# Optimization experiments

Measured on AMD Instinct MI355X. Metric: run time of the kernel, lower is better.

The kernel has to match this reference:

```python
import jax, jax.numpy as jnp
import numpy as np
import math

B, S_TGT, S_SRC, D, H, FF = 4, 2048, 2048, 512, 8, 2048
DK = D // H
EPS = 1e-6


def layernorm(x, gamma, mu):
    # torch: gamma*(x-mean)/(std+eps)+mu with unbiased std (ddof=1), eps OUTSIDE sqrt
    mean = jnp.mean(x, axis=-1, keepdims=True)
    std = jnp.std(x, axis=-1, keepdims=True, ddof=1)
    return gamma * (x - mean) / (std + EPS) + mu


def mha(q, k, v, wq, wk, wv, wo, bo, mask):
    # q:[B,Sq,D] k,v:[B,Sk,D]; weights [D,D] (applied as x@W)
    Bq, Sq, _ = q.shape
    Sk = k.shape[1]
    Q = (q @ wq).reshape(Bq, Sq, H, DK).transpose(0, 2, 1, 3)  # [B,H,Sq,dk]
    K = (k @ wk).reshape(Bq, Sk, H, DK).transpose(0, 2, 1, 3)
    V = (v @ wv).reshape(Bq, Sk, H, DK).transpose(0, 2, 1, 3)
    scores = jnp.einsum('bhqd,bhkd->bhqk', Q, K) / math.sqrt(DK)
    scores = jnp.where(mask == 0, -1e9, scores)
    attn = jax.nn.softmax(scores, axis=-1)
    out = jnp.einsum('bhqk,bhkd->bhqd', attn, V)  # [B,H,Sq,dk]
    out = out.transpose(0, 2, 1, 3).reshape(Bq, Sq, D)
    return out @ wo + bo


def setup_inputs() -> dict:
    key = jax.random.key(0)
    ks = jax.random.split(key, 20)
    sc = 0.02
    inp = {
        'x': jax.random.normal(ks[0], (B, S_TGT, D), jnp.float32),
        'encoder_output': jax.random.normal(ks[1], (B, S_SRC, D), jnp.float32),
        'src_mask': jnp.ones((1, 1, 1, S_SRC), jnp.int32),
        'tgt_mask': jnp.tril(jnp.ones((S_TGT, S_TGT), jnp.int32))[None, None],
        # self-attention params
        'sa_wq': jax.random.normal(ks[2], (D, D)) * sc,
        'sa_wk': jax.random.normal(ks[3], (D, D)) * sc,
        'sa_wv': jax.random.normal(ks[4], (D, D)) * sc,
        'sa_wo': jax.random.normal(ks[5], (D, D)) * sc,
        'sa_bo': jnp.zeros((D,), jnp.float32),
        # cross-attention params
        'ca_wq': jax.random.normal(ks[6], (D, D)) * sc,
        'ca_wk': jax.random.normal(ks[7], (D, D)) * sc,
        'ca_wv': jax.random.normal(ks[8], (D, D)) * sc,
        'ca_wo': jax.random.normal(ks[9], (D, D)) * sc,
        'ca_bo': jnp.zeros((D,), jnp.float32),
        # feed-forward params
        'ff_w1': jax.random.normal(ks[10], (D, FF)) * sc,
        'ff_b1': jnp.zeros((FF,), jnp.float32),
        'ff_w2': jax.random.normal(ks[11], (FF, D)) * sc,
        'ff_b2': jnp.zeros((D,), jnp.float32),
        # layernorm params (3 residual connections)
        'ln0_g': jnp.ones((D,), jnp.float32), 'ln0_b': jnp.zeros((D,), jnp.float32),
        'ln1_g': jnp.ones((D,), jnp.float32), 'ln1_b': jnp.zeros((D,), jnp.float32),
        'ln2_g': jnp.ones((D,), jnp.float32), 'ln2_b': jnp.zeros((D,), jnp.float32),
    }
    return inp


def reference(x, encoder_output, src_mask, tgt_mask,
              sa_wq, sa_wk, sa_wv, sa_wo, sa_bo,
              ca_wq, ca_wk, ca_wv, ca_wo, ca_bo,
              ff_w1, ff_b1, ff_w2, ff_b2,
              ln0_g, ln0_b, ln1_g, ln1_b, ln2_g, ln2_b):
    # pre-LN residual blocks; dropout in eval mode (identity)
    h = layernorm(x, ln0_g, ln0_b)
    x = x + mha(h, h, h, sa_wq, sa_wk, sa_wv, sa_wo, sa_bo, tgt_mask)
    h = layernorm(x, ln1_g, ln1_b)
    x = x + mha(h, encoder_output, encoder_output, ca_wq, ca_wk, ca_wv, ca_wo, ca_bo, src_mask)
    h = layernorm(x, ln2_g, ln2_b)
    ff = jax.nn.relu(h @ ff_w1 + ff_b1) @ ff_w2 + ff_b2
    return x + ff
```

## Files before the change

### kernel.cpp

```cpp
#include <hip/hip_runtime.h>
#include <cstdint>

typedef short s8v __attribute__((ext_vector_type(8)));
typedef short s4v __attribute__((ext_vector_type(4)));
typedef float f4v __attribute__((ext_vector_type(4)));
typedef unsigned int u32;

#define DEV static __device__ __forceinline__

DEV unsigned short f2bf(float f) {
  u32 u = __builtin_bit_cast(u32, f);
  u += 0x7FFF + ((u >> 16) & 1);
  return (unsigned short)(u >> 16);
}

DEV void gload16(const void* g, void* l) {
  __builtin_amdgcn_global_load_lds(
      (const __attribute__((address_space(1))) u32*)g,
      (__attribute__((address_space(3))) u32*)l, 16, 0, 0);
}

struct TransArgs {
  const float* in[10];
  unsigned short* out[10];
};

__global__ __launch_bounds__(256) void trans_all_kernel(TransArgs ta) {
  int id = blockIdx.x;
  int wi, t, K, N, tx, ty;
  if (id < 2048) {
    wi = id >> 8; t = id & 255; K = 512; N = 512; tx = t & 15; ty = t >> 4;
  } else if (id < 3072) {
    wi = 8; t = id - 2048; K = 512; N = 2048; tx = t & 63; ty = t >> 6;
  } else {
    wi = 9; t = id - 3072; K = 2048; N = 512; tx = t & 15; ty = t >> 4;
  }
  const float* in = ta.in[wi];
  unsigned short* out = ta.out[wi];
  __shared__ float tile[32][33];
  int lx = threadIdx.x & 31, ly = threadIdx.x >> 5;
  int bn = tx * 32, bk = ty * 32;
#pragma unroll
  for (int i = 0; i < 32; i += 8)
    tile[ly + i][lx] = in[(size_t)(bk + ly + i) * N + bn + lx];
  __syncthreads();
#pragma unroll
  for (int i = 0; i < 32; i += 8)
    out[(size_t)(bn + ly + i) * K + bk + lx] = f2bf(tile[lx][ly + i]);
}

__global__ __launch_bounds__(256) void cast_kernel(
    const float* __restrict__ in, unsigned short* __restrict__ out, int n8) {
  int i = blockIdx.x * 256 + threadIdx.x;
  if (i >= n8) return;
  const float4* p = (const float4*)(in + (size_t)i * 8);
  float4 a = p[0], b = p[1];
  float va[8] = {a.x, a.y, a.z, a.w, b.x, b.y, b.z, b.w};
  s8v o;
#pragma unroll
  for (int j = 0; j < 8; j++) o[j] = (short)f2bf(va[j]);
  *(s8v*)(out + (size_t)i * 8) = o;
}

__global__ __launch_bounds__(256) void ln_kernel(
    const float* __restrict__ x, const float* __restrict__ g,
    const float* __restrict__ bt, unsigned short* __restrict__ out) {
  int row = blockIdx.x * 4 + (threadIdx.x >> 6);
  int lane = threadIdx.x & 63;
  const float* xr = x + (size_t)row * 512 + lane * 8;
  float4 v0 = *(const float4*)xr;
  float4 v1 = *(const float4*)(xr + 4);
  float va[8] = {v0.x, v0.y, v0.z, v0.w, v1.x, v1.y, v1.z, v1.w};
  float s = 0.f, s2 = 0.f;
#pragma unroll
  for (int j = 0; j < 8; j++) { s += va[j]; s2 += va[j] * va[j]; }
#pragma unroll
  for (int off = 1; off < 64; off <<= 1) {
    s += __shfl_xor(s, off);
    s2 += __shfl_xor(s2, off);
  }
  float mean = s * (1.f / 512.f);
  float var = (s2 - 512.f * mean * mean) * (1.f / 511.f);
  var = fmaxf(var, 0.f);
  float inv = 1.f / (sqrtf(var) + 1e-6f);
  const float* gp = g + lane * 8;
  const float* bp = bt + lane * 8;
  float4 g0 = *(const float4*)gp, g1 = *(const float4*)(gp + 4);
  float4 b0 = *(const float4*)bp, b1 = *(const float4*)(bp + 4);
  float ga[8] = {g0.x, g0.y, g0.z, g0.w, g1.x, g1.y, g1.z, g1.w};
  float ba[8] = {b0.x, b0.y, b0.z, b0.w, b1.x, b1.y, b1.z, b1.w};
  s8v o;
#pragma unroll
  for (int j = 0; j < 8; j++)
    o[j] = (short)f2bf(ga[j] * (va[j] - mean) * inv + ba[j]);
  *(s8v*)(out + (size_t)row * 512 + lane * 8) = o;
}

#define EPI_QKV3 0
#define EPI_Q 1
#define EPI_KV2 2
#define EPI_BIAS_RES 3
#define EPI_RELU 4

template <int EPI, int BN>
__global__ __launch_bounds__(256, 3) void gemm_kernel(
    const unsigned short* __restrict__ A, const unsigned short* __restrict__ Bt,
    const float* __restrict__ bias, const float* __restrict__ res,
    void* __restrict__ out0, void* __restrict__ out1, void* __restrict__ out2,
    int M, int N, int K) {
  __shared__ alignas(16) unsigned short sA[2][128 * 32];
  __shared__ alignas(16) unsigned short sB[2][BN * 32];
  constexpr int NC = BN / 32;
  int tid = threadIdx.x;
  int w = tid >> 6, lane = tid & 63;
  int wm = w >> 1, wn = w & 1;
  int quad = lane >> 4, l15 = lane & 15;
  int bm = blockIdx.y * 128, bn = blockIdx.x * BN;

  int r0 = lane >> 2, c0 = (lane & 3) * 8;
  const unsigned short* gA0 = A + (size_t)(bm + w * 16 + r0) * K + c0;
  const unsigned short* gA1 = gA0 + (size_t)64 * K;
  const unsigned short* gB0 = Bt + (size_t)(bn + w * 16 + r0) * K + c0;
  const unsigned short* gB1 = gB0 + (size_t)64 * K;

  auto prefetch = [&](int k0, int buf) {
    gload16(gA0 + k0, &sA[buf][w * 512]);
    gload16(gA1 + k0, &sA[buf][(w + 4) * 512]);
    gload16(gB0 + k0, &sB[buf][w * 512]);
    if (BN == 128) gload16(gB1 + k0, &sB[buf][(w + 4) * 512]);
  };

  f4v acc[4][NC];
#pragma unroll
  for (int r = 0; r < 4; r++)
#pragma unroll
    for (int c = 0; c < NC; c++) acc[r][c] = {0.f, 0.f, 0.f, 0.f};

  prefetch(0, 0);
  int nk = K >> 5;
  for (int it = 0; it < nk; it++) {
    int buf = it & 1;
    __syncthreads();
    if (it + 1 < nk) prefetch((it + 1) << 5, buf ^ 1);
    s8v af[4], bf[NC];
#pragma unroll
    for (int r = 0; r < 4; r++)
      af[r] = *(const s8v*)&sA[buf][(wm * 64 + r * 16 + l15) * 32 + quad * 8];
#pragma unroll
    for (int c = 0; c < NC; c++)
      bf[c] = *(const s8v*)&sB[buf][(wn * (BN / 2) + c * 16 + l15) * 32 + quad * 8];
#pragma unroll
    for (int r = 0; r < 4; r++)
#pragma unroll
      for (int c = 0; c < NC; c++)
        acc[r][c] = __builtin_amdgcn_mfma_f32_16x16x32_bf16(af[r], bf[c], acc[r][c], 0, 0, 0);
  }

  constexpr int BP = 512 / BN;
  int route = 0;
  if (EPI == EPI_QKV3) route = blockIdx.x / BP;
  if (EPI == EPI_KV2) route = 1 + blockIdx.x / BP;
#pragma unroll
  for (int r = 0; r < 4; r++) {
#pragma unroll
    for (int c = 0; c < NC; c++) {
#pragma unroll
      for (int i = 0; i < 4; i++) {
        int row = bm + wm * 64 + r * 16 + quad * 4 + i;
        int col = bn + wn * (BN / 2) + c * 16 + l15;
        float v = acc[r][c][i];
        if (EPI == EPI_BIAS_RES) {
          float* o = (float*)out0;
          o[(size_t)row * N + col] = v + bias[col] + res[(size_t)row * N + col];
        } else if (EPI == EPI_RELU) {
          unsigned short* o = (unsigned short*)out0;
          o[(size_t)row * N + col] = f2bf(fmaxf(v + bias[col], 0.f));
        } else {
          int colq = col & 511;
          int b = row >> 11, s = row & 2047, h = colq >> 6, dk = colq & 63;
          if (route == 0) {
            unsigned short* o = (unsigned short*)out0;
            o[(((size_t)(b * 8 + h) * 2048) + s) * 64 + dk] = f2bf(v * 0.125f);
          } else if (route == 1) {
            unsigned short* o = (unsigned short*)out1;
            o[(((size_t)(b * 8 + h) * 2048) + s) * 64 + dk] = f2bf(v);
          } else {
            unsigned short* o = (unsigned short*)out2;
            o[(((size_t)(b * 8 + h) * 64) + dk) * 2048 + s] = f2bf(v);
          }
        }
      }
    }
  }
}

template <int CAUSAL>
__global__ __launch_bounds__(256, 2) void attn_kernel(
    const unsigned short* __restrict__ Q, const unsigned short* __restrict__ Kk,
    const unsigned short* __restrict__ Vt,
    unsigned short* __restrict__ out) {
  const int S = 2048;
  __shared__ alignas(16) unsigned short sK[2][64 * 64];
  __shared__ alignas(16) unsigned short sV[2][64 * 64];
  __shared__ alignas(16) unsigned short sO[128 * 68];
  int bh = blockIdx.x;
  int qt = CAUSAL ? ((int)gridDim.y - 1 - blockIdx.y) : blockIdx.y;
  int b = bh >> 3, h = bh & 7;
  int tid = threadIdx.x;
  int w = tid >> 6, lane = tid & 63;
  int quad = lane >> 4, l15 = lane & 15;

  const unsigned short* Qp = Q + (size_t)bh * S * 64;
  const unsigned short* Kp = Kk + (size_t)bh * S * 64;
  const unsigned short* Vp = Vt + (size_t)bh * 64 * S;

  s8v bq[2][2];
#pragma unroll
  for (int qb = 0; qb < 2; qb++) {
    const unsigned short* qr =
        Qp + (size_t)(qt * 128 + w * 32 + qb * 16 + l15) * 64 + quad * 8;
    bq[qb][0] = *(const s8v*)qr;
    bq[qb][1] = *(const s8v*)(qr + 32);
  }

  int rowA = ((l15 >> 2) * 8) + (l15 & 3);
  int koff[2][2][2];
#pragma unroll
  for (int win = 0; win < 2; win++)
#pragma unroll
    for (int half = 0; half < 2; half++) {
      int row = win * 32 + half * 4 + rowA;
      int h7 = (row & 7) ^ (((row >> 3) & 1) << 2);
      koff[win][half][0] = row * 64 + ((quad ^ h7) << 3);
      koff[win][half][1] = row * 64 + (((4 + quad) ^ h7) << 3);
    }
  int voff[4][2];
#pragma unroll
  for (int c2 = 0; c2 < 4; c2++) {
    int row = c2 * 16 + l15;
    int h7 = (row & 7) ^ (((row >> 3) & 1) << 2);
#pragma unroll
    for (int win = 0; win < 2; win++)
      voff[c2][win] = row * 64 + ((((win * 4) + quad) ^ h7) << 3);
  }
  int st_row[2], st_lds[2], st_cc[2];
#pragma unroll
  for (int c = 0; c < 2; c++) {
    int row = c * 32 + (tid >> 3), cc = tid & 7;
    int slot = cc ^ (row & 7) ^ (((row >> 3) & 1) << 2);
    st_row[c] = row;
    st_cc[c] = cc;
    st_lds[c] = row * 64 + slot * 8;
  }

  float l_lane[2] = {0.f, 0.f};
  f4v oacc[2][4];
#pragma unroll
  for (int qb = 0; qb < 2; qb++)
#pragma unroll
    for (int c2 = 0; c2 < 4; c2++) oacc[qb][c2] = {0.f, 0.f, 0.f, 0.f};

  int ntiles = CAUSAL ? (2 * qt + 2) : (S / 64);

  s8v kreg[2], vreg[2];
  auto load_t = [&](int t) {
    int kb = t * 64;
#pragma unroll
    for (int c = 0; c < 2; c++) {
      kreg[c] = *(const s8v*)(Kp + (size_t)(kb + st_row[c]) * 64 + st_cc[c] * 8);
      vreg[c] = *(const s8v*)(Vp + (size_t)st_row[c] * S + kb + st_cc[c] * 8);
    }
  };
  auto write_t = [&](int buf) {
#pragma unroll
    for (int c = 0; c < 2; c++) {
      *(s8v*)&sK[buf][st_lds[c]] = kreg[c];
      *(s8v*)&sV[buf][st_lds[c]] = vreg[c];
    }
  };

  load_t(0);
  write_t(0);

  for (int t = 0; t < ntiles; t++) {
    int buf = t & 1;
    __syncthreads();
    if (t + 1 < ntiles) load_t(t + 1);

    f4v sacc[2][2][2];
#pragma unroll
    for (int qb = 0; qb < 2; qb++)
#pragma unroll
      for (int win = 0; win < 2; win++)
#pragma unroll
        for (int half = 0; half < 2; half++) sacc[qb][win][half] = {0.f, 0.f, 0.f, 0.f};
#pragma unroll
    for (int win = 0; win < 2; win++)
#pragma unroll
      for (int half = 0; half < 2; half++) {
        s8v a0 = *(const s8v*)&sK[buf][koff[win][half][0]];
        s8v a1 = *(const s8v*)&sK[buf][koff[win][half][1]];
#pragma unroll
        for (int qb = 0; qb < 2; qb++) {
          sacc[qb][win][half] =
              __builtin_amdgcn_mfma_f32_16x16x32_bf16(a0, bq[qb][0], sacc[qb][win][half], 0, 0, 0);
          sacc[qb][win][half] =
              __builtin_amdgcn_mfma_f32_16x16x32_bf16(a1, bq[qb][1], sacc[qb][win][half], 0, 0, 0);
        }
      }

    if (CAUSAL && t >= 2 * qt) {
      int toff = (t - 2 * qt) * 64;
#pragma unroll
      for (int qb = 0; qb < 2; qb++) {
        int qloc = w * 32 + qb * 16 + l15;
#pragma unroll
        for (int win = 0; win < 2; win++)
#pragma unroll
          for (int half = 0; half < 2; half++)
#pragma unroll
            for (int i = 0; i < 4; i++)
              if (toff + win * 32 + quad * 8 + half * 4 + i > qloc)
                sacc[qb][win][half][i] = -1e9f;
      }
    }

    s8v bp[2][2];
#pragma unroll
    for (int qb = 0; qb < 2; qb++)
#pragma unroll
      for (int win = 0; win < 2; win++) {
        float p[8];
#pragma unroll
        for (int half = 0; half < 2; half++)
#pragma unroll
          for (int i = 0; i < 4; i++) {
            float e = __expf(sacc[qb][win][half][i]);
            p[half * 4 + i] = e;
            l_lane[qb] += e;
          }
        int4 pk;
#pragma unroll
        for (int j = 0; j < 4; j++)
          pk[j] = (int)__builtin_amdgcn_perm(
              __builtin_bit_cast(u32, p[2 * j + 1]),
              __builtin_bit_cast(u32, p[2 * j]), 0x07060302u);
        bp[qb][win] = __builtin_bit_cast(s8v, pk);
      }

#pragma unroll
    for (int c2 = 0; c2 < 4; c2++)
#pragma unroll
      for (int win = 0; win < 2; win++) {
        s8v av = *(const s8v*)&sV[buf][voff[c2][win]];
#pragma unroll
        for (int qb = 0; qb < 2; qb++)
          oacc[qb][c2] =
              __builtin_amdgcn_mfma_f32_16x16x32_bf16(av, bp[qb][win], oacc[qb][c2], 0, 0, 0);
      }

    if (t + 1 < ntiles) write_t(buf ^ 1);
  }

#pragma unroll
  for (int qb = 0; qb < 2; qb++) {
    float l = l_lane[qb];
    l += __shfl_xor(l, 16);
    l += __shfl_xor(l, 32);
    float inv = 1.f / l;
#pragma unroll
    for (int c2 = 0; c2 < 4; c2++) {
      s4v o;
#pragma unroll
      for (int i = 0; i < 4; i++) o[i] = (short)f2bf(oacc[qb][c2][i] * inv);
      *(s4v*)&sO[(w * 32 + qb * 16 + l15) * 68 + c2 * 16 + quad * 4] = o;
    }
  }
  __syncthreads();
#pragma unroll
  for (int c = 0; c < 4; c++) {
    int idx = c * 256 + tid;
    int r = idx >> 3, ch = idx & 7;
    s8v v = *(const s8v*)&sO[r * 68 + ch * 8];
    *(s8v*)(out + ((size_t)(b * S + qt * 128 + r) * 512) + h * 64 + ch * 8) = v;
  }
}

extern "C" void kernel_launch(void* const* d_in, const int* in_sizes, int n_in,
                              void* d_out, int out_size, void* d_ws, size_t ws_size,
                              hipStream_t stream) {
  const float* x = (const float*)d_in[0];
  const float* enc = (const float*)d_in[1];
  const float* sa_wq = (const float*)d_in[4];
  const float* sa_wk = (const float*)d_in[5];
  const float* sa_wv = (const float*)d_in[6];
  const float* sa_wo = (const float*)d_in[7];
  const float* sa_bo = (const float*)d_in[8];
  const float* ca_wq = (const float*)d_in[9];
  const float* ca_wk = (const float*)d_in[10];
  const float* ca_wv = (const float*)d_in[11];
  const float* ca_wo = (const float*)d_in[12];
  const float* ca_bo = (const float*)d_in[13];
  const float* ff_w1 = (const float*)d_in[14];
  const float* ff_b1 = (const float*)d_in[15];
  const float* ff_w2 = (const float*)d_in[16];
  const float* ff_b2 = (const float*)d_in[17];
  const float* ln0_g = (const float*)d_in[18];
  const float* ln0_b = (const float*)d_in[19];
  const float* ln1_g = (const float*)d_in[20];
  const float* ln1_b = (const float*)d_in[21];
  const float* ln2_g = (const float*)d_in[22];
  const float* ln2_b = (const float*)d_in[23];
  float* out = (float*)d_out;

  const int M = 8192;

  size_t off = 0;
  auto carve = [&](size_t bytes) -> void* {
    void* r = (char*)d_ws + off;
    off += (bytes + 255) & ~(size_t)255;
    return r;
  };
  unsigned short* swqT = (unsigned short*)carve(512 * 512 * 2);
  unsigned short* swkT = (unsigned short*)carve(512 * 512 * 2);
  unsigned short* swvT = (unsigned short*)carve(512 * 512 * 2);
  unsigned short* swoT = (unsigned short*)carve(512 * 512 * 2);
  unsigned short* cwqT = (unsigned short*)carve(512 * 512 * 2);
  unsigned short* cwkT = (unsigned short*)carve(512 * 512 * 2);
  unsigned short* cwvT = (unsigned short*)carve(512 * 512 * 2);
  unsigned short* cwoT = (unsigned short*)carve(512 * 512 * 2);
  unsigned short* w1T = (unsigned short*)carve((size_t)2048 * 512 * 2);
  unsigned short* w2T = (unsigned short*)carve((size_t)512 * 2048 * 2);
  unsigned short* enc_bf = (unsigned short*)carve((size_t)M * 512 * 2);
  unsigned short* h_bf = (unsigned short*)carve((size_t)M * 512 * 2);
  unsigned short* Qb = (unsigned short*)carve((size_t)M * 512 * 2);
  unsigned short* Kb = (unsigned short*)carve((size_t)M * 512 * 2);
  unsigned short* Vtb = (unsigned short*)carve((size_t)M * 512 * 2);
  unsigned short* attn_bf = (unsigned short*)carve((size_t)M * 512 * 2);
  float* x1 = (float*)carve((size_t)M * 512 * 4);
  unsigned short* f1 = (unsigned short*)carve((size_t)M * 2048 * 2);

  dim3 blk(256);

  TransArgs ta;
  ta.in[0] = sa_wq; ta.out[0] = swqT;
  ta.in[1] = sa_wk; ta.out[1] = swkT;
  ta.in[2] = sa_wv; ta.out[2] = swvT;
  ta.in[3] = sa_wo; ta.out[3] = swoT;
  ta.in[4] = ca_wq; ta.out[4] = cwqT;
  ta.in[5] = ca_wk; ta.out[5] = cwkT;
  ta.in[6] = ca_wv; ta.out[6] = cwvT;
  ta.in[7] = ca_wo; ta.out[7] = cwoT;
  ta.in[8] = ff_w1; ta.out[8] = w1T;
  ta.in[9] = ff_w2; ta.out[9] = w2T;
  trans_all_kernel<<<dim3(4096), blk, 0, stream>>>(ta);
  cast_kernel<<<dim3(M * 512 / 8 / 256), blk, 0, stream>>>(enc, enc_bf, M * 512 / 8);

  dim3 gProj(8, 64);
  dim3 gQKV(12, 64);
  dim3 gKV(16, 64);
  dim3 gFF1(16, 64);
  dim3 gAttn(32, 16);
  dim3 gLN(M / 4);

  ln_kernel<<<gLN, blk, 0, stream>>>(x, ln0_g, ln0_b, h_bf);
  gemm_kernel<EPI_QKV3, 128><<<gQKV, blk, 0, stream>>>(h_bf, swqT, nullptr, nullptr, Qb, Kb, Vtb, M, 1536, 512);
  attn_kernel<1><<<gAttn, blk, 0, stream>>>(Qb, Kb, Vtb, attn_bf);
  gemm_kernel<EPI_BIAS_RES, 64><<<gProj, blk, 0, stream>>>(attn_bf, swoT, sa_bo, x, x1, nullptr, nullptr, M, 512, 512);

  ln_kernel<<<gLN, blk, 0, stream>>>(x1, ln1_g, ln1_b, h_bf);
  gemm_kernel<EPI_Q, 64><<<gProj, blk, 0, stream>>>(h_bf, cwqT, nullptr, nullptr, Qb, nullptr, nullptr, M, 512, 512);
  gemm_kernel<EPI_KV2, 64><<<gKV, blk, 0, stream>>>(enc_bf, cwkT, nullptr, nullptr, nullptr, Kb, Vtb, M, 1024, 512);
  attn_kernel<0><<<gAttn, blk, 0, stream>>>(Qb, Kb, Vtb, attn_bf);
  gemm_kernel<EPI_BIAS_RES, 64><<<gProj, blk, 0, stream>>>(attn_bf, cwoT, ca_bo, x1, x1, nullptr, nullptr, M, 512, 512);

  ln_kernel<<<gLN, blk, 0, stream>>>(x1, ln2_g, ln2_b, h_bf);
  gemm_kernel<EPI_RELU, 128><<<gFF1, blk, 0, stream>>>(h_bf, w1T, ff_b1, nullptr, f1, nullptr, nullptr, M, 2048, 512);
  gemm_kernel<EPI_BIAS_RES, 64><<<gProj, blk, 0, stream>>>(f1, w2T, ff_b2, x1, out, nullptr, nullptr, M, 512, 2048);
}
```

Measured before the change: 415.6 us.

## Deepen attention K/V register prefetch, use exp2 softmax, swizzle GEMM blocks per XCD

The attention loop now keeps two register sets of K/V tiles and is unrolled by two, so global loads are issued two tiles ahead and more memory latency is hidden. The Q scale folds in log2(e), which lets softmax use exp2 in place of expf. The GEMM block index is remapped so consecutive row tiles are grouped per XCD, aiming for better L2 reuse of the A rows. The cost is higher register pressure in the attention kernel. The two-tile loop also assumes ntiles is even, which holds for the causal and full cases here.

```diff
diff --git a/kernel.cpp b/kernel.cpp
--- a/kernel.cpp
+++ b/kernel.cpp
@@ -101,6 +101,8 @@
 #define EPI_KV2 2
 #define EPI_BIAS_RES 3
 #define EPI_RELU 4
+
+#define QSCALE 0.18033688f
 
 template <int EPI, int BN>
 __global__ __launch_bounds__(256, 3) void gemm_kernel(
@@ -115,7 +117,12 @@
   int w = tid >> 6, lane = tid & 63;
   int wm = w >> 1, wn = w & 1;
   int quad = lane >> 4, l15 = lane & 15;
-  int bm = blockIdx.y * 128, bn = blockIdx.x * BN;
+
+  int lin = blockIdx.x + gridDim.x * blockIdx.y;
+  int xcd = lin & 7, j = lin >> 3;
+  int bmi = xcd * 8 + (j & 7);
+  int bni = j >> 3;
+  int bm = bmi * 128, bn = bni * BN;
 
   int r0 = lane >> 2, c0 = (lane & 3) * 8;
   const unsigned short* gA0 = A + (size_t)(bm + w * 16 + r0) * K + c0;
@@ -158,8 +165,8 @@
 
   constexpr int BP = 512 / BN;
   int route = 0;
-  if (EPI == EPI_QKV3) route = blockIdx.x / BP;
-  if (EPI == EPI_KV2) route = 1 + blockIdx.x / BP;
+  if (EPI == EPI_QKV3) route = bni / BP;
+  if (EPI == EPI_KV2) route = 1 + bni / BP;
 #pragma unroll
   for (int r = 0; r < 4; r++) {
 #pragma unroll
@@ -180,7 +187,7 @@
           int b = row >> 11, s = row & 2047, h = colq >> 6, dk = colq & 63;
           if (route == 0) {
             unsigned short* o = (unsigned short*)out0;
-            o[(((size_t)(b * 8 + h) * 2048) + s) * 64 + dk] = f2bf(v * 0.125f);
+            o[(((size_t)(b * 8 + h) * 2048) + s) * 64 + dk] = f2bf(v * QSCALE);
           } else if (route == 1) {
             unsigned short* o = (unsigned short*)out1;
             o[(((size_t)(b * 8 + h) * 2048) + s) * 64 + dk] = f2bf(v);
@@ -262,31 +269,24 @@
 
   int ntiles = CAUSAL ? (2 * qt + 2) : (S / 64);
 
-  s8v kreg[2], vreg[2];
-  auto load_t = [&](int t) {
+  s8v rk[2][2], rv[2][2];
+  auto load_set = [&](int t, int set) {
     int kb = t * 64;
 #pragma unroll
     for (int c = 0; c < 2; c++) {
-      kreg[c] = *(const s8v*)(Kp + (size_t)(kb + st_row[c]) * 64 + st_cc[c] * 8);
-      vreg[c] = *(const s8v*)(Vp + (size_t)st_row[c] * S + kb + st_cc[c] * 8);
+      rk[set][c] = *(const s8v*)(Kp + (size_t)(kb + st_row[c]) * 64 + st_cc[c] * 8);
+      rv[set][c] = *(const s8v*)(Vp + (size_t)st_row[c] * S + kb + st_cc[c] * 8);
     }
   };
-  auto write_t = [&](int buf) {
+  auto write_set = [&](int buf, int set) {
 #pragma unroll
     for (int c = 0; c < 2; c++) {
-      *(s8v*)&sK[buf][st_lds[c]] = kreg[c];
-      *(s8v*)&sV[buf][st_lds[c]] = vreg[c];
+      *(s8v*)&sK[buf][st_lds[c]] = rk[set][c];
+      *(s8v*)&sV[buf][st_lds[c]] = rv[set][c];
     }
   };
 
-  load_t(0);
-  write_t(0);
-
-  for (int t = 0; t < ntiles; t++) {
-    int buf = t & 1;
-    __syncthreads();
-    if (t + 1 < ntiles) load_t(t + 1);
-
+  auto compute = [&](int buf, int t) {
     f4v sacc[2][2][2];
 #pragma unroll
     for (int qb = 0; qb < 2; qb++)
@@ -335,16 +335,16 @@
         for (int half = 0; half < 2; half++)
 #pragma unroll
           for (int i = 0; i < 4; i++) {
-            float e = __expf(sacc[qb][win][half][i]);
+            float e = __builtin_exp2f(sacc[qb][win][half][i]);
             p[half * 4 + i] = e;
             l_lane[qb] += e;
           }
         int4 pk;
 #pragma unroll
-        for (int j = 0; j < 4; j++)
-          pk[j] = (int)__builtin_amdgcn_perm(
-              __builtin_bit_cast(u32, p[2 * j + 1]),
-              __builtin_bit_cast(u32, p[2 * j]), 0x07060302u);
+        for (int jj = 0; jj < 4; jj++)
+          pk[jj] = (int)__builtin_amdgcn_perm(
+              __builtin_bit_cast(u32, p[2 * jj + 1]),
+              __builtin_bit_cast(u32, p[2 * jj]), 0x07060302u);
         bp[qb][win] = __builtin_bit_cast(s8v, pk);
       }
 
@@ -358,8 +358,21 @@
           oacc[qb][c2] =
               __builtin_amdgcn_mfma_f32_16x16x32_bf16(av, bp[qb][win], oacc[qb][c2], 0, 0, 0);
       }
-
-    if (t + 1 < ntiles) write_t(buf ^ 1);
+  };
+
+  load_set(0, 0);
+  write_set(0, 0);
+  load_set(1, 1);
+
+  for (int t = 0; t < ntiles; t += 2) {
+    __syncthreads();
+    if (t + 2 < ntiles) load_set(t + 2, 0);
+    compute(0, t);
+    write_set(1, 1);
+    __syncthreads();
+    if (t + 3 < ntiles) load_set(t + 3, 1);
+    compute(1, t + 1);
+    if (t + 2 < ntiles) write_set(0, 0);
   }
 
 #pragma unroll
```

After: 392.7 us. 5.5% less time.
